# Kernel optimization log

Measured on AMD Instinct MI355X. Metric: run time of the kernel, lower is better.

The kernel has to match this reference:

```python
import jax, jax.numpy as jnp
import numpy as np
import math

D_MODEL, N_HEADS, D_HEAD = 1024, 16, 64
INIT_RANGE = 0.02
IGNORE = -100000.0


def setup_inputs() -> dict:
    key = jax.random.key(0)
    ks = jax.random.split(key, 5)
    x = jax.random.normal(ks[0], (2, 2048, D_MODEL), dtype=jnp.float32)
    W_Q = INIT_RANGE * jax.random.normal(ks[1], (N_HEADS, D_MODEL, D_HEAD), dtype=jnp.float32)
    W_K = INIT_RANGE * jax.random.normal(ks[2], (N_HEADS, D_MODEL, D_HEAD), dtype=jnp.float32)
    W_V = INIT_RANGE * jax.random.normal(ks[3], (N_HEADS, D_MODEL, D_HEAD), dtype=jnp.float32)
    # W_O is contracted as 'n_heads d_head d_model' in the original einsum
    W_O = INIT_RANGE * jax.random.normal(ks[4], (N_HEADS, D_HEAD, D_MODEL), dtype=jnp.float32)
    b_Q = jnp.zeros((N_HEADS, D_HEAD), dtype=jnp.float32)
    b_K = jnp.zeros((N_HEADS, D_HEAD), dtype=jnp.float32)
    b_V = jnp.zeros((N_HEADS, D_HEAD), dtype=jnp.float32)
    b_O = jnp.zeros((D_MODEL,), dtype=jnp.float32)
    return {"normalized_resid_pre": x, "W_Q": W_Q, "b_Q": b_Q, "W_K": W_K, "b_K": b_K,
            "W_V": W_V, "b_V": b_V, "W_O": W_O, "b_O": b_O}


def reference(normalized_resid_pre, W_Q, b_Q, W_K, b_K, W_V, b_V, W_O, b_O):
    x = normalized_resid_pre  # [b, s, d_model]
    q = jnp.einsum('bsd,hde->bshe', x, W_Q) + b_Q  # [b, s, h, d_head]
    k = jnp.einsum('bsd,hde->bshe', x, W_K) + b_K
    v = jnp.einsum('bsd,hde->bshe', x, W_V) + b_V
    scores = jnp.einsum('bqhe,bkhe->bhqk', q, k) / math.sqrt(D_HEAD)
    S = x.shape[1]
    causal = jnp.tril(jnp.ones((S, S), dtype=bool))  # True where allowed
    scores = jnp.where(causal, scores, IGNORE)
    pattern = jax.nn.softmax(scores, axis=-1)  # [b, h, q, k]
    z = jnp.einsum('bhqk,bkhe->bqhe', pattern, v)
    attn_out = jnp.einsum('bqhe,hed->bqd', z, W_O) + b_O
    return attn_out
```

## Files before the change

### kernel.cpp

```cpp
#include <hip/hip_runtime.h>
#include <cstdint>
#include <cstddef>

typedef unsigned short u16;
typedef __bf16 bf16x8 __attribute__((ext_vector_type(8)));
typedef _Float16 f16x4 __attribute__((ext_vector_type(4)));
typedef _Float16 f16x2 __attribute__((ext_vector_type(2)));
typedef float  f32x4  __attribute__((ext_vector_type(4)));
typedef unsigned short u16x8 __attribute__((ext_vector_type(8)));
typedef unsigned short u16x4 __attribute__((ext_vector_type(4)));

#define DM   1024
#define NH   16
#define DH   64
#define SS   2048
#define BSZ  4096
#define NQKV 3072
#define QSCALE 0.18033688011f

__device__ __forceinline__ u16 f2b(float f) {
  unsigned u = __builtin_bit_cast(unsigned, f);
  return (u16)((u + 0x7FFFu + ((u >> 16) & 1u)) >> 16);
}
__device__ __forceinline__ u16 f2h(float f) {
  _Float16 h = (_Float16)f;
  return __builtin_bit_cast(u16, h);
}

__device__ __forceinline__ void gl_lds16(const void* g, void* l) {
  __builtin_amdgcn_global_load_lds(
      (__attribute__((address_space(1))) void*)(void*)g,
      (__attribute__((address_space(3))) void*)l, 16, 0, 0);
}

__global__ __launch_bounds__(256) void prep_all_kernel(
    const float* __restrict__ x, u16* __restrict__ xb,
    const float* __restrict__ Wq, const float* __restrict__ Wk,
    const float* __restrict__ Wv, u16* __restrict__ wqkvt,
    const float* __restrict__ Wo, u16* __restrict__ wot) {
  __shared__ __align__(16) u16 Ts[64 * 72];
  int bid = blockIdx.x, t = threadIdx.x;
  if (bid < 2048) {
    int i = (bid * 256 + t) * 8;
    float4 a = *(const float4*)(x + i);
    float4 b = *(const float4*)(x + i + 4);
    u16x8 o;
    o[0] = f2b(a.x); o[1] = f2b(a.y); o[2] = f2b(a.z); o[3] = f2b(a.w);
    o[4] = f2b(b.x); o[5] = f2b(b.y); o[6] = f2b(b.z); o[7] = f2b(b.w);
    *(u16x8*)(xb + i) = o;
    return;
  }
  if (bid < 2816) {
    int idx = bid - 2048;
    int dt = idx & 15, sl = idx >> 4;
    int proj = sl >> 4, h = sl & 15;
    const float* W = (proj == 0) ? Wq : ((proj == 1) ? Wk : Wv);
    int d0 = dt * 64;
    {
      int ld = t >> 2;
      int ec = (t & 3) * 16;
      const float* src = W + ((size_t)h * DM + d0 + ld) * DH + ec;
      float4 v0 = *(const float4*)(src);
      float4 v1 = *(const float4*)(src + 4);
      float4 v2 = *(const float4*)(src + 8);
      float4 v3 = *(const float4*)(src + 12);
      float vv[16] = {v0.x, v0.y, v0.z, v0.w, v1.x, v1.y, v1.z, v1.w,
                      v2.x, v2.y, v2.z, v2.w, v3.x, v3.y, v3.z, v3.w};
#pragma unroll
      for (int i = 0; i < 16; i++) Ts[(ec + i) * 72 + ld] = f2b(vv[i]);
    }
    __syncthreads();
    {
      int le = t >> 2;
      int dc = (t & 3) * 16;
      int n = proj * DM + h * DH + le;
      u16* dst = wqkvt + (size_t)n * DM + d0 + dc;
      *(u16x8*)(dst)     = *(const u16x8*)&Ts[le * 72 + dc];
      *(u16x8*)(dst + 8) = *(const u16x8*)&Ts[le * 72 + dc + 8];
    }
    return;
  }
  {
    int idx = bid - 2816;
    int dt = idx & 15, h = idx >> 4;
    int d0 = dt * 64;
    {
      int le = t >> 2;
      int dc = (t & 3) * 16;
      const float* src = Wo + ((size_t)h * DH + le) * DM + d0 + dc;
      float4 v0 = *(const float4*)(src);
      float4 v1 = *(const float4*)(src + 4);
      float4 v2 = *(const float4*)(src + 8);
      float4 v3 = *(const float4*)(src + 12);
      float vv[16] = {v0.x, v0.y, v0.z, v0.w, v1.x, v1.y, v1.z, v1.w,
                      v2.x, v2.y, v2.z, v2.w, v3.x, v3.y, v3.z, v3.w};
#pragma unroll
      for (int i = 0; i < 16; i++) Ts[(dc + i) * 72 + le] = f2b(vv[i]);
    }
    __syncthreads();
    {
      int ld = t >> 2;
      int ec = (t & 3) * 16;
      u16* dst = wot + (size_t)(d0 + ld) * DM + h * DH + ec;
      *(u16x8*)(dst)     = *(const u16x8*)&Ts[ld * 72 + ec];
      *(u16x8*)(dst + 8) = *(const u16x8*)&Ts[ld * 72 + ec + 8];
    }
  }
}

__global__ __launch_bounds__(256) void gemm_qkv_kernel(
    const u16* __restrict__ A, const u16* __restrict__ Bt,
    u16* __restrict__ o_q, u16* __restrict__ o_k, u16* __restrict__ o_v,
    const float* __restrict__ c0, const float* __restrict__ c1,
    const float* __restrict__ c2) {
  const int K = DM;
  __shared__ __align__(16) u16 As[128 * 32];
  __shared__ __align__(16) u16 Bs[128 * 32];
  __shared__ __align__(16) u16 Cs[64 * 128];
  int t = threadIdx.x, w = t >> 6, l = t & 63;
  int lr = l & 15, lq = l >> 4;
  int m0 = blockIdx.x * 128, n0 = blockIdx.y * 128;
  int wr = w >> 1, wc = w & 1;
  f32x4 acc[4][4] = {};
  const u16* ga = A + (size_t)(m0 + (t >> 2)) * K + (t & 3) * 8;
  const u16* gb = Bt + (size_t)(n0 + (t >> 2)) * K + (t & 3) * 8;

  for (int k0 = 0; k0 < K; k0 += 32) {
    __syncthreads();
    gl_lds16(ga + k0,           &As[w * 512]);
    gl_lds16(ga + k0 + 64 * K,  &As[2048 + w * 512]);
    gl_lds16(gb + k0,           &Bs[w * 512]);
    gl_lds16(gb + k0 + 64 * K,  &Bs[2048 + w * 512]);
    __syncthreads();
    bf16x8 af[4], bfr[4];
#pragma unroll
    for (int i = 0; i < 4; i++)
      af[i] = *(const bf16x8*)&As[(wr * 64 + i * 16 + lr) * 32 + lq * 8];
#pragma unroll
    for (int j = 0; j < 4; j++)
      bfr[j] = *(const bf16x8*)&Bs[(wc * 64 + j * 16 + lr) * 32 + lq * 8];
#pragma unroll
    for (int i = 0; i < 4; i++)
#pragma unroll
      for (int j = 0; j < 4; j++)
        acc[i][j] = __builtin_amdgcn_mfma_f32_16x16x32_bf16(af[i], bfr[j], acc[i][j], 0, 0, 0);
  }

  int proj = n0 >> 10;
  int r0 = n0 & 1023;
  int h0 = r0 >> 6;
  const float* bp = (proj == 0) ? c0 : ((proj == 1) ? c1 : c2);

#pragma unroll
  for (int p = 0; p < 2; p++) {
    __syncthreads();
    if (wr == p) {
#pragma unroll
      for (int j = 0; j < 4; j++) {
        int nl = wc * 64 + j * 16 + lr;
        float bias = bp[r0 + nl];
#pragma unroll
        for (int i = 0; i < 4; i++) {
#pragma unroll
          for (int g = 0; g < 4; g++) {
            int ml = i * 16 + lq * 4 + g;
            float val = acc[i][j][g] + bias;
            if (proj == 0)      Cs[ml * 128 + nl] = f2b(val * QSCALE);
            else if (proj == 1) Cs[ml * 128 + nl] = f2b(val);
            else                Cs[nl * 64 + ml] = f2h(val);
          }
        }
      }
    }
    __syncthreads();
    int m_base = m0 + p * 64;
    if (proj < 2) {
      int ml = t >> 2, q4 = t & 3;
      int hh = q4 >> 1, e0 = (q4 & 1) * 32;
      int m = m_base + ml, b = m >> 11, s = m & 2047;
      int h = h0 + hh;
      u16* dst = (proj == 0 ? o_q : o_k) + ((size_t)(b * NH + h) * SS + s) * DH + e0;
      const u16* src = &Cs[ml * 128 + hh * 64 + e0];
      *(u16x8*)(dst)      = *(const u16x8*)(src);
      *(u16x8*)(dst + 8)  = *(const u16x8*)(src + 8);
      *(u16x8*)(dst + 16) = *(const u16x8*)(src + 16);
      *(u16x8*)(dst + 24) = *(const u16x8*)(src + 24);
    } else {
      int er = t >> 1, sh = t & 1;
      int hh = er >> 6, e = er & 63;
      int h = h0 + hh;
      int ms = m_base + sh * 32, b = ms >> 11, s = ms & 2047;
      u16* dst = o_v + ((size_t)(b * NH + h) * DH + e) * SS + s;
      const u16* src = &Cs[er * 64 + sh * 32];
      *(u16x8*)(dst)      = *(const u16x8*)(src);
      *(u16x8*)(dst + 8)  = *(const u16x8*)(src + 8);
      *(u16x8*)(dst + 16) = *(const u16x8*)(src + 16);
      *(u16x8*)(dst + 24) = *(const u16x8*)(src + 24);
    }
  }
}

__global__ __launch_bounds__(256) void gemm_o_kernel(
    const u16* __restrict__ A, const u16* __restrict__ Bt,
    const float* __restrict__ bo, float* __restrict__ fout) {
  const int K = DM;
  __shared__ __align__(16) u16 As[128 * 32];
  __shared__ __align__(16) u16 Bs[64 * 32];
  int t = threadIdx.x, w = t >> 6, l = t & 63;
  int lr = l & 15, lq = l >> 4;
  int m0 = blockIdx.x * 128, n0 = blockIdx.y * 64;
  f32x4 acc[2][4] = {};
  const u16* ga = A + (size_t)(m0 + (t >> 2)) * K + (t & 3) * 8;
  const u16* gb = Bt + (size_t)(n0 + (t >> 2)) * K + (t & 3) * 8;

  for (int k0 = 0; k0 < K; k0 += 32) {
    __syncthreads();
    gl_lds16(ga + k0,           &As[w * 512]);
    gl_lds16(ga + k0 + 64 * K,  &As[2048 + w * 512]);
    gl_lds16(gb + k0, &Bs[w * 512]);
    __syncthreads();
    bf16x8 af[2], bfr[4];
#pragma unroll
    for (int i = 0; i < 2; i++)
      af[i] = *(const bf16x8*)&As[(w * 32 + i * 16 + lr) * 32 + lq * 8];
#pragma unroll
    for (int j = 0; j < 4; j++)
      bfr[j] = *(const bf16x8*)&Bs[(j * 16 + lr) * 32 + lq * 8];
#pragma unroll
    for (int i = 0; i < 2; i++)
#pragma unroll
      for (int j = 0; j < 4; j++)
        acc[i][j] = __builtin_amdgcn_mfma_f32_16x16x32_bf16(af[i], bfr[j], acc[i][j], 0, 0, 0);
  }

  int mb = m0 + w * 32 + lq * 4;
  int nb = n0 + lr;
#pragma unroll
  for (int j = 0; j < 4; j++) {
    int n = nb + j * 16;
    float bias = bo[n];
#pragma unroll
    for (int i = 0; i < 2; i++) {
#pragma unroll
      for (int g = 0; g < 4; g++) {
        int m = mb + i * 16 + g;
        fout[(size_t)m * DM + n] = acc[i][j][g] + bias;
      }
    }
  }
}

__global__ __launch_bounds__(128) void attn_kernel(const u16* __restrict__ q_ws,
                                                   const u16* __restrict__ k_ws,
                                                   const u16* __restrict__ vt_ws,
                                                   u16* __restrict__ z_ws) {
  __shared__ __align__(16) u16 Ks[2][64 * 72], Vs[2][64 * 72];

  int t = threadIdx.x;
  int w = t >> 6;
  int l = t & 63;
  int lr = l & 15, lq = l >> 4;
  int srow = t >> 3;
  int sc8 = (t & 7) * 8;

  int bid = blockIdx.x;
  int xcd = bid & 7, idx = bid >> 3;
  int bh = xcd * 4 + (idx & 3);
  int p = idx >> 2;
  int bq = p & 7, quad = p >> 3;
  int qt = (quad == 0) ? bq : (quad == 1) ? (15 - bq)
         : (quad == 2) ? (16 + bq) : (31 - bq);
  const u16* Qb = q_ws + (size_t)bh * SS * DH;
  const u16* Kb = k_ws + (size_t)bh * SS * DH;
  const u16* Vb = vt_ws + (size_t)bh * DH * SS;
  int b = bh >> 4, h16 = bh & 15;

  int q0 = qt * 64;
  int nkt = qt + 1;

  int qr0 = q0 + w * 32 + lr;
  bf16x8 qf00 = *(const bf16x8*)(Qb + (size_t)qr0 * DH + lq * 8);
  bf16x8 qf01 = *(const bf16x8*)(Qb + (size_t)qr0 * DH + 32 + lq * 8);
  bf16x8 qf10 = *(const bf16x8*)(Qb + (size_t)(qr0 + 16) * DH + lq * 8);
  bf16x8 qf11 = *(const bf16x8*)(Qb + (size_t)(qr0 + 16) * DH + 32 + lq * 8);

  f32x4 accO0[4] = {}, accO1[4] = {};
  float accL0 = 0.f, accL1 = 0.f;

  {
    const u16* kg = Kb + (size_t)srow * DH + sc8;
    const u16* vg = Vb + (size_t)srow * SS + sc8;
#pragma unroll
    for (int j2 = 0; j2 < 4; j2++) {
      *(u16x8*)&Ks[0][(srow + 16 * j2) * 72 + sc8] = *(const u16x8*)(kg + 16 * j2 * DH);
      *(u16x8*)&Vs[0][(srow + 16 * j2) * 72 + sc8] = *(const u16x8*)(vg + (size_t)16 * j2 * SS);
    }
  }

  for (int it = 0; it < nkt; ++it) {
    __syncthreads();
    int pb = it & 1;
    bool have_next = (it + 1 < nkt);

    u16x8 rk[4], rv[4];
    if (have_next) {
      int k0n = (it + 1) * 64;
      const u16* kg = Kb + (size_t)(k0n + srow) * DH + sc8;
      const u16* vg = Vb + (size_t)srow * SS + k0n + sc8;
#pragma unroll
      for (int j2 = 0; j2 < 4; j2++) {
        rk[j2] = *(const u16x8*)(kg + 16 * j2 * DH);
        rv[j2] = *(const u16x8*)(vg + (size_t)16 * j2 * SS);
      }
    }

    f32x4 sc0[4], sc1[4];
#pragma unroll
    for (int nt = 0; nt < 4; nt++) {
      bf16x8 kf0 = *(const bf16x8*)&Ks[pb][(nt * 16 + lr) * 72 + lq * 8];
      bf16x8 kf1 = *(const bf16x8*)&Ks[pb][(nt * 16 + lr) * 72 + 32 + lq * 8];
      f32x4 a = {0.f, 0.f, 0.f, 0.f};
      a = __builtin_amdgcn_mfma_f32_16x16x32_bf16(kf0, qf00, a, 0, 0, 0);
      a = __builtin_amdgcn_mfma_f32_16x16x32_bf16(kf1, qf01, a, 0, 0, 0);
      sc0[nt] = a;
      f32x4 c = {0.f, 0.f, 0.f, 0.f};
      c = __builtin_amdgcn_mfma_f32_16x16x32_bf16(kf0, qf10, c, 0, 0, 0);
      c = __builtin_amdgcn_mfma_f32_16x16x32_bf16(kf1, qf11, c, 0, 0, 0);
      sc1[nt] = c;
    }

    if (it == nkt - 1) {
      int k0 = it * 64;
#pragma unroll
      for (int nt = 0; nt < 4; nt++) {
#pragma unroll
        for (int gg = 0; gg < 4; gg++) {
          int gk = k0 + nt * 16 + lq * 4 + gg;
          if (gk > qr0) sc0[nt][gg] = -1e30f;
          if (gk > qr0 + 16) sc1[nt][gg] = -1e30f;
        }
      }
    }

    f16x4 pf0[4], pf1[4];
#pragma unroll
    for (int nt = 0; nt < 4; nt++) {
      float a0 = __builtin_amdgcn_exp2f(sc0[nt][0]);
      float a1 = __builtin_amdgcn_exp2f(sc0[nt][1]);
      float a2 = __builtin_amdgcn_exp2f(sc0[nt][2]);
      float a3 = __builtin_amdgcn_exp2f(sc0[nt][3]);
      accL0 += (a0 + a1) + (a2 + a3);
      f16x2 e0 = __builtin_bit_cast(f16x2, __builtin_amdgcn_cvt_pkrtz(a0, a1));
      f16x2 e1 = __builtin_bit_cast(f16x2, __builtin_amdgcn_cvt_pkrtz(a2, a3));
      pf0[nt][0] = e0[0]; pf0[nt][1] = e0[1];
      pf0[nt][2] = e1[0]; pf0[nt][3] = e1[1];
      float c0v = __builtin_amdgcn_exp2f(sc1[nt][0]);
      float c1v = __builtin_amdgcn_exp2f(sc1[nt][1]);
      float c2v = __builtin_amdgcn_exp2f(sc1[nt][2]);
      float c3v = __builtin_amdgcn_exp2f(sc1[nt][3]);
      accL1 += (c0v + c1v) + (c2v + c3v);
      f16x2 e2 = __builtin_bit_cast(f16x2, __builtin_amdgcn_cvt_pkrtz(c0v, c1v));
      f16x2 e3 = __builtin_bit_cast(f16x2, __builtin_amdgcn_cvt_pkrtz(c2v, c3v));
      pf1[nt][0] = e2[0]; pf1[nt][1] = e2[1];
      pf1[nt][2] = e3[0]; pf1[nt][3] = e3[1];
    }

#pragma unroll
    for (int ks = 0; ks < 4; ks++) {
#pragma unroll
      for (int et = 0; et < 4; et++) {
        f16x4 vf = *(const f16x4*)&Vs[pb][(et * 16 + lr) * 72 + ks * 16 + lq * 4];
        accO0[et] = __builtin_amdgcn_mfma_f32_16x16x16f16(vf, pf0[ks], accO0[et], 0, 0, 0);
        accO1[et] = __builtin_amdgcn_mfma_f32_16x16x16f16(vf, pf1[ks], accO1[et], 0, 0, 0);
      }
    }

    if (have_next) {
      int nb = (it + 1) & 1;
#pragma unroll
      for (int j2 = 0; j2 < 4; j2++) {
        *(u16x8*)&Ks[nb][(srow + 16 * j2) * 72 + sc8] = rk[j2];
        *(u16x8*)&Vs[nb][(srow + 16 * j2) * 72 + sc8] = rv[j2];
      }
    }
  }

  accL0 += __shfl_xor(accL0, 16, 64);
  accL0 += __shfl_xor(accL0, 32, 64);
  accL1 += __shfl_xor(accL1, 16, 64);
  accL1 += __shfl_xor(accL1, 32, 64);
  float inv0 = 1.0f / accL0;
  float inv1 = 1.0f / accL1;

  u16* zrow0 = z_ws + ((size_t)(b * SS + qr0)) * DM + h16 * DH;
  u16* zrow1 = z_ws + ((size_t)(b * SS + qr0 + 16)) * DM + h16 * DH;
#pragma unroll
  for (int et = 0; et < 4; et++) {
    u16x4 o0, o1;
#pragma unroll
    for (int gg = 0; gg < 4; gg++) {
      o0[gg] = f2b(accO0[et][gg] * inv0);
      o1[gg] = f2b(accO1[et][gg] * inv1);
    }
    *(u16x4*)(zrow0 + et * 16 + lq * 4) = o0;
    *(u16x4*)(zrow1 + et * 16 + lq * 4) = o1;
  }
}

extern "C" void kernel_launch(void* const* d_in, const int* in_sizes, int n_in,
                              void* d_out, int out_size, void* d_ws, size_t ws_size,
                              hipStream_t stream) {
  const float* x  = (const float*)d_in[0];
  const float* Wq = (const float*)d_in[1];
  const float* bq = (const float*)d_in[2];
  const float* Wk = (const float*)d_in[3];
  const float* bk = (const float*)d_in[4];
  const float* Wv = (const float*)d_in[5];
  const float* bv = (const float*)d_in[6];
  const float* Wo = (const float*)d_in[7];
  const float* bo = (const float*)d_in[8];
  float* out = (float*)d_out;

  char* ws = (char*)d_ws;
  const size_t MB = 1u << 20;
  u16* xb    = (u16*)(ws);
  u16* wqkvt = (u16*)(ws + 8 * MB);
  u16* wot   = (u16*)(ws + 14 * MB);
  u16* q_ws  = (u16*)(ws + 16 * MB);
  u16* k_ws  = (u16*)(ws + 24 * MB);
  u16* vt_ws = (u16*)(ws + 32 * MB);
  u16* z_ws  = (u16*)(ws + 40 * MB);

  prep_all_kernel<<<3072, 256, 0, stream>>>(x, xb, Wq, Wk, Wv, wqkvt, Wo, wot);

  gemm_qkv_kernel<<<dim3(BSZ / 128, NQKV / 128), 256, 0, stream>>>(
      xb, wqkvt, q_ws, k_ws, vt_ws, bq, bk, bv);

  attn_kernel<<<1024, 128, 0, stream>>>(q_ws, k_ws, vt_ws, z_ws);

  gemm_o_kernel<<<dim3(BSZ / 128, DM / 64), 256, 0, stream>>>(z_ws, wot, bo, out);
}
```

Measured before the change: 186.4 us.

## Double-buffer LDS tiles in QKV and output GEMMs to overlap loads with MFMA

```diff
diff --git a/kernel.cpp b/kernel.cpp
--- a/kernel.cpp
+++ b/kernel.cpp
@@ -114,9 +114,8 @@
     const float* __restrict__ c0, const float* __restrict__ c1,
     const float* __restrict__ c2) {
   const int K = DM;
-  __shared__ __align__(16) u16 As[128 * 32];
-  __shared__ __align__(16) u16 Bs[128 * 32];
-  __shared__ __align__(16) u16 Cs[64 * 128];
+  __shared__ __align__(16) u16 AB[2][2][128 * 32];
+  u16* Cs = &AB[0][0][0];
   int t = threadIdx.x, w = t >> 6, l = t & 63;
   int lr = l & 15, lq = l >> 4;
   int m0 = blockIdx.x * 128, n0 = blockIdx.y * 128;
@@ -125,25 +124,40 @@
   const u16* ga = A + (size_t)(m0 + (t >> 2)) * K + (t & 3) * 8;
   const u16* gb = Bt + (size_t)(n0 + (t >> 2)) * K + (t & 3) * 8;
 
-  for (int k0 = 0; k0 < K; k0 += 32) {
-    __syncthreads();
-    gl_lds16(ga + k0,           &As[w * 512]);
-    gl_lds16(ga + k0 + 64 * K,  &As[2048 + w * 512]);
-    gl_lds16(gb + k0,           &Bs[w * 512]);
-    gl_lds16(gb + k0 + 64 * K,  &Bs[2048 + w * 512]);
-    __syncthreads();
+  gl_lds16(ga,          &AB[0][0][w * 512]);
+  gl_lds16(ga + 64 * K, &AB[0][0][2048 + w * 512]);
+  gl_lds16(gb,          &AB[0][1][w * 512]);
+  gl_lds16(gb + 64 * K, &AB[0][1][2048 + w * 512]);
+
+#pragma unroll 2
+  for (int it = 0; it < 32; ++it) {
+    int cur = it & 1;
+    if (it + 1 < 32) {
+      int kn = it * 32 + 32;
+      gl_lds16(ga + kn,          &AB[cur ^ 1][0][w * 512]);
+      gl_lds16(ga + kn + 64 * K, &AB[cur ^ 1][0][2048 + w * 512]);
+      gl_lds16(gb + kn,          &AB[cur ^ 1][1][w * 512]);
+      gl_lds16(gb + kn + 64 * K, &AB[cur ^ 1][1][2048 + w * 512]);
+      asm volatile("s_waitcnt vmcnt(4)" ::: "memory");
+    } else {
+      asm volatile("s_waitcnt vmcnt(0)" ::: "memory");
+    }
+    __builtin_amdgcn_s_barrier();
+    __builtin_amdgcn_sched_barrier(0);
     bf16x8 af[4], bfr[4];
 #pragma unroll
     for (int i = 0; i < 4; i++)
-      af[i] = *(const bf16x8*)&As[(wr * 64 + i * 16 + lr) * 32 + lq * 8];
+      af[i] = *(const bf16x8*)&AB[cur][0][(wr * 64 + i * 16 + lr) * 32 + lq * 8];
 #pragma unroll
     for (int j = 0; j < 4; j++)
-      bfr[j] = *(const bf16x8*)&Bs[(wc * 64 + j * 16 + lr) * 32 + lq * 8];
+      bfr[j] = *(const bf16x8*)&AB[cur][1][(wc * 64 + j * 16 + lr) * 32 + lq * 8];
 #pragma unroll
     for (int i = 0; i < 4; i++)
 #pragma unroll
       for (int j = 0; j < 4; j++)
         acc[i][j] = __builtin_amdgcn_mfma_f32_16x16x32_bf16(af[i], bfr[j], acc[i][j], 0, 0, 0);
+    __builtin_amdgcn_sched_barrier(0);
+    __builtin_amdgcn_s_barrier();
   }
 
   int proj = n0 >> 10;
@@ -204,8 +218,8 @@
     const u16* __restrict__ A, const u16* __restrict__ Bt,
     const float* __restrict__ bo, float* __restrict__ fout) {
   const int K = DM;
-  __shared__ __align__(16) u16 As[128 * 32];
-  __shared__ __align__(16) u16 Bs[64 * 32];
+  __shared__ __align__(16) u16 As[2][128 * 32];
+  __shared__ __align__(16) u16 Bs[2][64 * 32];
   int t = threadIdx.x, w = t >> 6, l = t & 63;
   int lr = l & 15, lq = l >> 4;
   int m0 = blockIdx.x * 128, n0 = blockIdx.y * 64;
@@ -213,24 +227,38 @@
   const u16* ga = A + (size_t)(m0 + (t >> 2)) * K + (t & 3) * 8;
   const u16* gb = Bt + (size_t)(n0 + (t >> 2)) * K + (t & 3) * 8;
 
-  for (int k0 = 0; k0 < K; k0 += 32) {
-    __syncthreads();
-    gl_lds16(ga + k0,           &As[w * 512]);
-    gl_lds16(ga + k0 + 64 * K,  &As[2048 + w * 512]);
-    gl_lds16(gb + k0, &Bs[w * 512]);
-    __syncthreads();
+  gl_lds16(ga,          &As[0][w * 512]);
+  gl_lds16(ga + 64 * K, &As[0][2048 + w * 512]);
+  gl_lds16(gb,          &Bs[0][w * 512]);
+
+#pragma unroll 2
+  for (int it = 0; it < 32; ++it) {
+    int cur = it & 1;
+    if (it + 1 < 32) {
+      int kn = it * 32 + 32;
+      gl_lds16(ga + kn,          &As[cur ^ 1][w * 512]);
+      gl_lds16(ga + kn + 64 * K, &As[cur ^ 1][2048 + w * 512]);
+      gl_lds16(gb + kn,          &Bs[cur ^ 1][w * 512]);
+      asm volatile("s_waitcnt vmcnt(3)" ::: "memory");
+    } else {
+      asm volatile("s_waitcnt vmcnt(0)" ::: "memory");
+    }
+    __builtin_amdgcn_s_barrier();
+    __builtin_amdgcn_sched_barrier(0);
     bf16x8 af[2], bfr[4];
 #pragma unroll
     for (int i = 0; i < 2; i++)
-      af[i] = *(const bf16x8*)&As[(w * 32 + i * 16 + lr) * 32 + lq * 8];
+      af[i] = *(const bf16x8*)&As[cur][(w * 32 + i * 16 + lr) * 32 + lq * 8];
 #pragma unroll
     for (int j = 0; j < 4; j++)
-      bfr[j] = *(const bf16x8*)&Bs[(j * 16 + lr) * 32 + lq * 8];
+      bfr[j] = *(const bf16x8*)&Bs[cur][(j * 16 + lr) * 32 + lq * 8];
 #pragma unroll
     for (int i = 0; i < 2; i++)
 #pragma unroll
       for (int j = 0; j < 4; j++)
         acc[i][j] = __builtin_amdgcn_mfma_f32_16x16x32_bf16(af[i], bfr[j], acc[i][j], 0, 0, 0);
+    __builtin_amdgcn_sched_barrier(0);
+    __builtin_amdgcn_s_barrier();
   }
 
   int mb = m0 + w * 32 + lq * 4;
```

After: 189.9 us. Within noise of the previous version (+1.9%).

## Deepen GEMM K-tiles to 64 with XOR-swizzled LDS and add MFMA priority hints

Applied to the files above, without the earlier changes.

```diff
diff --git a/kernel.cpp b/kernel.cpp
--- a/kernel.cpp
+++ b/kernel.cpp
@@ -114,36 +114,43 @@
     const float* __restrict__ c0, const float* __restrict__ c1,
     const float* __restrict__ c2) {
   const int K = DM;
-  __shared__ __align__(16) u16 As[128 * 32];
-  __shared__ __align__(16) u16 Bs[128 * 32];
-  __shared__ __align__(16) u16 Cs[64 * 128];
+  __shared__ __align__(16) u16 As[128 * 64];
+  __shared__ __align__(16) u16 Bs[128 * 64];
+  u16* Cs = As;
   int t = threadIdx.x, w = t >> 6, l = t & 63;
   int lr = l & 15, lq = l >> 4;
   int m0 = blockIdx.x * 128, n0 = blockIdx.y * 128;
   int wr = w >> 1, wc = w & 1;
   f32x4 acc[4][4] = {};
-  const u16* ga = A + (size_t)(m0 + (t >> 2)) * K + (t & 3) * 8;
-  const u16* gb = Bt + (size_t)(n0 + (t >> 2)) * K + (t & 3) * 8;
-
-  for (int k0 = 0; k0 < K; k0 += 32) {
-    __syncthreads();
-    gl_lds16(ga + k0,           &As[w * 512]);
-    gl_lds16(ga + k0 + 64 * K,  &As[2048 + w * 512]);
-    gl_lds16(gb + k0,           &Bs[w * 512]);
-    gl_lds16(gb + k0 + 64 * K,  &Bs[2048 + w * 512]);
-    __syncthreads();
-    bf16x8 af[4], bfr[4];
-#pragma unroll
-    for (int i = 0; i < 4; i++)
-      af[i] = *(const bf16x8*)&As[(wr * 64 + i * 16 + lr) * 32 + lq * 8];
-#pragma unroll
-    for (int j = 0; j < 4; j++)
-      bfr[j] = *(const bf16x8*)&Bs[(wc * 64 + j * 16 + lr) * 32 + lq * 8];
-#pragma unroll
-    for (int i = 0; i < 4; i++)
-#pragma unroll
-      for (int j = 0; j < 4; j++)
-        acc[i][j] = __builtin_amdgcn_mfma_f32_16x16x32_bf16(af[i], bfr[j], acc[i][j], 0, 0, 0);
+  int srow = t >> 3;
+  int sslot = (t & 7) ^ (srow & 7);
+  const u16* ga = A + (size_t)(m0 + srow) * K + sslot * 8;
+  const u16* gb = Bt + (size_t)(n0 + srow) * K + sslot * 8;
+  int rsw = lr & 7;
+
+  for (int k0 = 0; k0 < K; k0 += 64) {
+    __syncthreads();
+#pragma unroll
+    for (int o = 0; o < 4; o++) {
+      gl_lds16(ga + k0 + (size_t)(o * 32) * K, &As[o * 2048 + w * 512]);
+      gl_lds16(gb + k0 + (size_t)(o * 32) * K, &Bs[o * 2048 + w * 512]);
+    }
+    __syncthreads();
+#pragma unroll
+    for (int ks = 0; ks < 2; ks++) {
+      int slot = ((ks * 4 + lq) ^ rsw) * 8;
+      bf16x8 af[4], bfr[4];
+#pragma unroll
+      for (int i = 0; i < 4; i++) {
+        af[i]  = *(const bf16x8*)&As[(wr * 64 + i * 16 + lr) * 64 + slot];
+        bfr[i] = *(const bf16x8*)&Bs[(wc * 64 + i * 16 + lr) * 64 + slot];
+      }
+#pragma unroll
+      for (int i = 0; i < 4; i++)
+#pragma unroll
+        for (int j = 0; j < 4; j++)
+          acc[i][j] = __builtin_amdgcn_mfma_f32_16x16x32_bf16(af[i], bfr[j], acc[i][j], 0, 0, 0);
+    }
   }
 
   int proj = n0 >> 10;
@@ -204,33 +211,43 @@
     const u16* __restrict__ A, const u16* __restrict__ Bt,
     const float* __restrict__ bo, float* __restrict__ fout) {
   const int K = DM;
-  __shared__ __align__(16) u16 As[128 * 32];
-  __shared__ __align__(16) u16 Bs[64 * 32];
+  __shared__ __align__(16) u16 As[128 * 64];
+  __shared__ __align__(16) u16 Bs[64 * 64];
   int t = threadIdx.x, w = t >> 6, l = t & 63;
   int lr = l & 15, lq = l >> 4;
   int m0 = blockIdx.x * 128, n0 = blockIdx.y * 64;
   f32x4 acc[2][4] = {};
-  const u16* ga = A + (size_t)(m0 + (t >> 2)) * K + (t & 3) * 8;
-  const u16* gb = Bt + (size_t)(n0 + (t >> 2)) * K + (t & 3) * 8;
-
-  for (int k0 = 0; k0 < K; k0 += 32) {
-    __syncthreads();
-    gl_lds16(ga + k0,           &As[w * 512]);
-    gl_lds16(ga + k0 + 64 * K,  &As[2048 + w * 512]);
-    gl_lds16(gb + k0, &Bs[w * 512]);
-    __syncthreads();
-    bf16x8 af[2], bfr[4];
-#pragma unroll
-    for (int i = 0; i < 2; i++)
-      af[i] = *(const bf16x8*)&As[(w * 32 + i * 16 + lr) * 32 + lq * 8];
-#pragma unroll
-    for (int j = 0; j < 4; j++)
-      bfr[j] = *(const bf16x8*)&Bs[(j * 16 + lr) * 32 + lq * 8];
-#pragma unroll
-    for (int i = 0; i < 2; i++)
+  int srow = t >> 3;
+  int sslot = (t & 7) ^ (srow & 7);
+  const u16* ga = A + (size_t)(m0 + srow) * K + sslot * 8;
+  const u16* gb = Bt + (size_t)(n0 + srow) * K + sslot * 8;
+  int rsw = lr & 7;
+
+  for (int k0 = 0; k0 < K; k0 += 64) {
+    __syncthreads();
+#pragma unroll
+    for (int o = 0; o < 4; o++)
+      gl_lds16(ga + k0 + (size_t)(o * 32) * K, &As[o * 2048 + w * 512]);
+#pragma unroll
+    for (int o = 0; o < 2; o++)
+      gl_lds16(gb + k0 + (size_t)(o * 32) * K, &Bs[o * 2048 + w * 512]);
+    __syncthreads();
+#pragma unroll
+    for (int ks = 0; ks < 2; ks++) {
+      int slot = ((ks * 4 + lq) ^ rsw) * 8;
+      bf16x8 af[2], bfr[4];
+#pragma unroll
+      for (int i = 0; i < 2; i++)
+        af[i] = *(const bf16x8*)&As[(w * 32 + i * 16 + lr) * 64 + slot];
 #pragma unroll
       for (int j = 0; j < 4; j++)
-        acc[i][j] = __builtin_amdgcn_mfma_f32_16x16x32_bf16(af[i], bfr[j], acc[i][j], 0, 0, 0);
+        bfr[j] = *(const bf16x8*)&Bs[(j * 16 + lr) * 64 + slot];
+#pragma unroll
+      for (int i = 0; i < 2; i++)
+#pragma unroll
+        for (int j = 0; j < 4; j++)
+          acc[i][j] = __builtin_amdgcn_mfma_f32_16x16x32_bf16(af[i], bfr[j], acc[i][j], 0, 0, 0);
+    }
   }
 
   int mb = m0 + w * 32 + lq * 4;
@@ -319,6 +336,7 @@
     for (int nt = 0; nt < 4; nt++) {
       bf16x8 kf0 = *(const bf16x8*)&Ks[pb][(nt * 16 + lr) * 72 + lq * 8];
       bf16x8 kf1 = *(const bf16x8*)&Ks[pb][(nt * 16 + lr) * 72 + 32 + lq * 8];
+      __builtin_amdgcn_s_setprio(1);
       f32x4 a = {0.f, 0.f, 0.f, 0.f};
       a = __builtin_amdgcn_mfma_f32_16x16x32_bf16(kf0, qf00, a, 0, 0, 0);
       a = __builtin_amdgcn_mfma_f32_16x16x32_bf16(kf1, qf01, a, 0, 0, 0);
@@ -327,6 +345,7 @@
       c = __builtin_amdgcn_mfma_f32_16x16x32_bf16(kf0, qf10, c, 0, 0, 0);
       c = __builtin_amdgcn_mfma_f32_16x16x32_bf16(kf1, qf11, c, 0, 0, 0);
       sc1[nt] = c;
+      __builtin_amdgcn_s_setprio(0);
     }
 
     if (it == nkt - 1) {
@@ -367,12 +386,17 @@
 
 #pragma unroll
     for (int ks = 0; ks < 4; ks++) {
+      f16x4 vfr[4];
+#pragma unroll
+      for (int et = 0; et < 4; et++)
+        vfr[et] = *(const f16x4*)&Vs[pb][(et * 16 + lr) * 72 + ks * 16 + lq * 4];
+      __builtin_amdgcn_s_setprio(1);
 #pragma unroll
       for (int et = 0; et < 4; et++) {
-        f16x4 vf = *(const f16x4*)&Vs[pb][(et * 16 + lr) * 72 + ks * 16 + lq * 4];
-        accO0[et] = __builtin_amdgcn_mfma_f32_16x16x16f16(vf, pf0[ks], accO0[et], 0, 0, 0);
-        accO1[et] = __builtin_amdgcn_mfma_f32_16x16x16f16(vf, pf1[ks], accO1[et], 0, 0, 0);
-      }
+        accO0[et] = __builtin_amdgcn_mfma_f32_16x16x16f16(vfr[et], pf0[ks], accO0[et], 0, 0, 0);
+        accO1[et] = __builtin_amdgcn_mfma_f32_16x16x16f16(vfr[et], pf1[ks], accO1[et], 0, 0, 0);
+      }
+      __builtin_amdgcn_s_setprio(0);
     }
 
     if (have_next) {
```

New measurement: 204.1 us. 1.09x slower.

## Use 128-row query tiles with 4 waves sharing K/V tiles in attention

Applied to the files above, without the earlier changes.

```diff
diff --git a/kernel.cpp b/kernel.cpp
--- a/kernel.cpp
+++ b/kernel.cpp
@@ -250,7 +250,7 @@
   }
 }
 
-__global__ __launch_bounds__(128) void attn_kernel(const u16* __restrict__ q_ws,
+__global__ __launch_bounds__(256) void attn_kernel(const u16* __restrict__ q_ws,
                                                    const u16* __restrict__ k_ws,
                                                    const u16* __restrict__ vt_ws,
                                                    u16* __restrict__ z_ws) {
@@ -267,16 +267,16 @@
   int xcd = bid & 7, idx = bid >> 3;
   int bh = xcd * 4 + (idx & 3);
   int p = idx >> 2;
-  int bq = p & 7, quad = p >> 3;
-  int qt = (quad == 0) ? bq : (quad == 1) ? (15 - bq)
-         : (quad == 2) ? (16 + bq) : (31 - bq);
+  int bq = p & 7;
+  int jt = (p >> 3) ? (15 - bq) : bq;
   const u16* Qb = q_ws + (size_t)bh * SS * DH;
   const u16* Kb = k_ws + (size_t)bh * SS * DH;
   const u16* Vb = vt_ws + (size_t)bh * DH * SS;
   int b = bh >> 4, h16 = bh & 15;
 
-  int q0 = qt * 64;
-  int nkt = qt + 1;
+  int q0 = jt * 128;
+  int nkt = 2 * jt + 2;
+  int my_last = nkt - 2 + (w >> 1);
 
   int qr0 = q0 + w * 32 + lr;
   bf16x8 qf00 = *(const bf16x8*)(Qb + (size_t)qr0 * DH + lq * 8);
@@ -290,11 +290,10 @@
   {
     const u16* kg = Kb + (size_t)srow * DH + sc8;
     const u16* vg = Vb + (size_t)srow * SS + sc8;
-#pragma unroll
-    for (int j2 = 0; j2 < 4; j2++) {
-      *(u16x8*)&Ks[0][(srow + 16 * j2) * 72 + sc8] = *(const u16x8*)(kg + 16 * j2 * DH);
-      *(u16x8*)&Vs[0][(srow + 16 * j2) * 72 + sc8] = *(const u16x8*)(vg + (size_t)16 * j2 * SS);
-    }
+    *(u16x8*)&Ks[0][srow * 72 + sc8] = *(const u16x8*)kg;
+    *(u16x8*)&Ks[0][(srow + 32) * 72 + sc8] = *(const u16x8*)(kg + 32 * DH);
+    *(u16x8*)&Vs[0][srow * 72 + sc8] = *(const u16x8*)vg;
+    *(u16x8*)&Vs[0][(srow + 32) * 72 + sc8] = *(const u16x8*)(vg + (size_t)32 * SS);
   }
 
   for (int it = 0; it < nkt; ++it) {
@@ -302,86 +301,93 @@
     int pb = it & 1;
     bool have_next = (it + 1 < nkt);
 
-    u16x8 rk[4], rv[4];
+    u16x8 rk0, rk1, rv0, rv1;
     if (have_next) {
       int k0n = (it + 1) * 64;
       const u16* kg = Kb + (size_t)(k0n + srow) * DH + sc8;
       const u16* vg = Vb + (size_t)srow * SS + k0n + sc8;
-#pragma unroll
-      for (int j2 = 0; j2 < 4; j2++) {
-        rk[j2] = *(const u16x8*)(kg + 16 * j2 * DH);
-        rv[j2] = *(const u16x8*)(vg + (size_t)16 * j2 * SS);
-      }
-    }
-
-    f32x4 sc0[4], sc1[4];
-#pragma unroll
-    for (int nt = 0; nt < 4; nt++) {
-      bf16x8 kf0 = *(const bf16x8*)&Ks[pb][(nt * 16 + lr) * 72 + lq * 8];
-      bf16x8 kf1 = *(const bf16x8*)&Ks[pb][(nt * 16 + lr) * 72 + 32 + lq * 8];
-      f32x4 a = {0.f, 0.f, 0.f, 0.f};
-      a = __builtin_amdgcn_mfma_f32_16x16x32_bf16(kf0, qf00, a, 0, 0, 0);
-      a = __builtin_amdgcn_mfma_f32_16x16x32_bf16(kf1, qf01, a, 0, 0, 0);
-      sc0[nt] = a;
-      f32x4 c = {0.f, 0.f, 0.f, 0.f};
-      c = __builtin_amdgcn_mfma_f32_16x16x32_bf16(kf0, qf10, c, 0, 0, 0);
-      c = __builtin_amdgcn_mfma_f32_16x16x32_bf16(kf1, qf11, c, 0, 0, 0);
-      sc1[nt] = c;
-    }
-
-    if (it == nkt - 1) {
-      int k0 = it * 64;
+      rk0 = *(const u16x8*)kg;
+      rk1 = *(const u16x8*)(kg + 32 * DH);
+      rv0 = *(const u16x8*)vg;
+      rv1 = *(const u16x8*)(vg + (size_t)32 * SS);
+    }
+
+    if (it <= my_last) {
+      f32x4 sc0[4], sc1[4];
 #pragma unroll
       for (int nt = 0; nt < 4; nt++) {
-#pragma unroll
-        for (int gg = 0; gg < 4; gg++) {
-          int gk = k0 + nt * 16 + lq * 4 + gg;
-          if (gk > qr0) sc0[nt][gg] = -1e30f;
-          if (gk > qr0 + 16) sc1[nt][gg] = -1e30f;
+        bf16x8 kf0 = *(const bf16x8*)&Ks[pb][(nt * 16 + lr) * 72 + lq * 8];
+        bf16x8 kf1 = *(const bf16x8*)&Ks[pb][(nt * 16 + lr) * 72 + 32 + lq * 8];
+        __builtin_amdgcn_s_setprio(1);
+        f32x4 a = {0.f, 0.f, 0.f, 0.f};
+        a = __builtin_amdgcn_mfma_f32_16x16x32_bf16(kf0, qf00, a, 0, 0, 0);
+        a = __builtin_amdgcn_mfma_f32_16x16x32_bf16(kf1, qf01, a, 0, 0, 0);
+        sc0[nt] = a;
+        f32x4 c = {0.f, 0.f, 0.f, 0.f};
+        c = __builtin_amdgcn_mfma_f32_16x16x32_bf16(kf0, qf10, c, 0, 0, 0);
+        c = __builtin_amdgcn_mfma_f32_16x16x32_bf16(kf1, qf11, c, 0, 0, 0);
+        sc1[nt] = c;
+        __builtin_amdgcn_s_setprio(0);
+      }
+
+      if (it == my_last) {
+        int k0 = it * 64;
+#pragma unroll
+        for (int nt = 0; nt < 4; nt++) {
+#pragma unroll
+          for (int gg = 0; gg < 4; gg++) {
+            int gk = k0 + nt * 16 + lq * 4 + gg;
+            if (gk > qr0) sc0[nt][gg] = -1e30f;
+            if (gk > qr0 + 16) sc1[nt][gg] = -1e30f;
+          }
         }
       }
-    }
-
-    f16x4 pf0[4], pf1[4];
-#pragma unroll
-    for (int nt = 0; nt < 4; nt++) {
-      float a0 = __builtin_amdgcn_exp2f(sc0[nt][0]);
-      float a1 = __builtin_amdgcn_exp2f(sc0[nt][1]);
-      float a2 = __builtin_amdgcn_exp2f(sc0[nt][2]);
-      float a3 = __builtin_amdgcn_exp2f(sc0[nt][3]);
-      accL0 += (a0 + a1) + (a2 + a3);
-      f16x2 e0 = __builtin_bit_cast(f16x2, __builtin_amdgcn_cvt_pkrtz(a0, a1));
-      f16x2 e1 = __builtin_bit_cast(f16x2, __builtin_amdgcn_cvt_pkrtz(a2, a3));
-      pf0[nt][0] = e0[0]; pf0[nt][1] = e0[1];
-      pf0[nt][2] = e1[0]; pf0[nt][3] = e1[1];
-      float c0v = __builtin_amdgcn_exp2f(sc1[nt][0]);
-      float c1v = __builtin_amdgcn_exp2f(sc1[nt][1]);
-      float c2v = __builtin_amdgcn_exp2f(sc1[nt][2]);
-      float c3v = __builtin_amdgcn_exp2f(sc1[nt][3]);
-      accL1 += (c0v + c1v) + (c2v + c3v);
-      f16x2 e2 = __builtin_bit_cast(f16x2, __builtin_amdgcn_cvt_pkrtz(c0v, c1v));
-      f16x2 e3 = __builtin_bit_cast(f16x2, __builtin_amdgcn_cvt_pkrtz(c2v, c3v));
-      pf1[nt][0] = e2[0]; pf1[nt][1] = e2[1];
-      pf1[nt][2] = e3[0]; pf1[nt][3] = e3[1];
-    }
-
-#pragma unroll
-    for (int ks = 0; ks < 4; ks++) {
-#pragma unroll
-      for (int et = 0; et < 4; et++) {
-        f16x4 vf = *(const f16x4*)&Vs[pb][(et * 16 + lr) * 72 + ks * 16 + lq * 4];
-        accO0[et] = __builtin_amdgcn_mfma_f32_16x16x16f16(vf, pf0[ks], accO0[et], 0, 0, 0);
-        accO1[et] = __builtin_amdgcn_mfma_f32_16x16x16f16(vf, pf1[ks], accO1[et], 0, 0, 0);
+
+      f16x4 pf0[4], pf1[4];
+#pragma unroll
+      for (int nt = 0; nt < 4; nt++) {
+        float a0 = __builtin_amdgcn_exp2f(sc0[nt][0]);
+        float a1 = __builtin_amdgcn_exp2f(sc0[nt][1]);
+        float a2 = __builtin_amdgcn_exp2f(sc0[nt][2]);
+        float a3 = __builtin_amdgcn_exp2f(sc0[nt][3]);
+        accL0 += (a0 + a1) + (a2 + a3);
+        f16x2 e0 = __builtin_bit_cast(f16x2, __builtin_amdgcn_cvt_pkrtz(a0, a1));
+        f16x2 e1 = __builtin_bit_cast(f16x2, __builtin_amdgcn_cvt_pkrtz(a2, a3));
+        pf0[nt][0] = e0[0]; pf0[nt][1] = e0[1];
+        pf0[nt][2] = e1[0]; pf0[nt][3] = e1[1];
+        float c0v = __builtin_amdgcn_exp2f(sc1[nt][0]);
+        float c1v = __builtin_amdgcn_exp2f(sc1[nt][1]);
+        float c2v = __builtin_amdgcn_exp2f(sc1[nt][2]);
+        float c3v = __builtin_amdgcn_exp2f(sc1[nt][3]);
+        accL1 += (c0v + c1v) + (c2v + c3v);
+        f16x2 e2 = __builtin_bit_cast(f16x2, __builtin_amdgcn_cvt_pkrtz(c0v, c1v));
+        f16x2 e3 = __builtin_bit_cast(f16x2, __builtin_amdgcn_cvt_pkrtz(c2v, c3v));
+        pf1[nt][0] = e2[0]; pf1[nt][1] = e2[1];
+        pf1[nt][2] = e3[0]; pf1[nt][3] = e3[1];
+      }
+
+#pragma unroll
+      for (int ks = 0; ks < 4; ks++) {
+        f16x4 vfr[4];
+#pragma unroll
+        for (int et = 0; et < 4; et++)
+          vfr[et] = *(const f16x4*)&Vs[pb][(et * 16 + lr) * 72 + ks * 16 + lq * 4];
+        __builtin_amdgcn_s_setprio(1);
+#pragma unroll
+        for (int et = 0; et < 4; et++) {
+          accO0[et] = __builtin_amdgcn_mfma_f32_16x16x16f16(vfr[et], pf0[ks], accO0[et], 0, 0, 0);
+          accO1[et] = __builtin_amdgcn_mfma_f32_16x16x16f16(vfr[et], pf1[ks], accO1[et], 0, 0, 0);
+        }
+        __builtin_amdgcn_s_setprio(0);
       }
     }
 
     if (have_next) {
       int nb = (it + 1) & 1;
-#pragma unroll
-      for (int j2 = 0; j2 < 4; j2++) {
-        *(u16x8*)&Ks[nb][(srow + 16 * j2) * 72 + sc8] = rk[j2];
-        *(u16x8*)&Vs[nb][(srow + 16 * j2) * 72 + sc8] = rv[j2];
-      }
+      *(u16x8*)&Ks[nb][srow * 72 + sc8] = rk0;
+      *(u16x8*)&Ks[nb][(srow + 32) * 72 + sc8] = rk1;
+      *(u16x8*)&Vs[nb][srow * 72 + sc8] = rv0;
+      *(u16x8*)&Vs[nb][(srow + 32) * 72 + sc8] = rv1;
     }
   }
 
@@ -436,7 +442,7 @@
   gemm_qkv_kernel<<<dim3(BSZ / 128, NQKV / 128), 256, 0, stream>>>(
       xb, wqkvt, q_ws, k_ws, vt_ws, bq, bk, bv);
 
-  attn_kernel<<<1024, 128, 0, stream>>>(q_ws, k_ws, vt_ws, z_ws);
+  attn_kernel<<<512, 256, 0, stream>>>(q_ws, k_ws, vt_ws, z_ws);
 
   gemm_o_kernel<<<dim3(BSZ / 128, DM / 64), 256, 0, stream>>>(z_ws, wot, bo, out);
 }
```

After: 190.1 us. No clear change (+2.0%).
